# Kernel optimization log

Measured on AMD Instinct MI355X. Metric: run time of the kernel, lower is better.

Reference implementation:

```python
import jax, jax.numpy as jnp
import numpy as np


def setup_inputs() -> dict:
    key = jax.random.key(0)
    k1, k2, k3 = jax.random.split(key, 3)
    B, H, W, C, Q = 32, 64, 64, 256, 4
    h = jax.random.normal(k1, (B, H, W, C), dtype=jnp.float32)
    mask = jax.random.randint(k2, (B, H, W), 0, 2) == 1  # True = masked out
    queries = jax.random.normal(k3, (Q, C), dtype=jnp.float32)
    return {"h": h, "mask": mask, "queries": queries}


def reference(h, mask, queries):
    B, H, W, C = h.shape
    Q = queries.shape[0]
    scale = C ** (-0.5)
    h_flat = h.reshape(B, H * W, C)            # [B, N, C]
    # scores: [B, Q, N]
    attn = jnp.einsum('qc,bnc->bqn', queries, h_flat) * scale
    mask_flat = mask.reshape(B, 1, H * W)      # True -> -inf
    attn = jnp.where(mask_flat, -jnp.inf, attn)
    attn = jax.nn.softmax(attn, axis=-1)
    attn = jnp.where(jnp.isnan(attn), 0.0, attn)  # nan_to_num for fully-masked rows
    pooled = jnp.einsum('bqn,bnc->bqc', attn, h_flat)
    return pooled.reshape(B, Q * C)
```

## Files before the change

### kernel.cpp

```cpp
#include <hip/hip_runtime.h>
#include <math.h>

#define QN  4
#define CN  256
#define BN  32
#define NN  4096
#define WV  4
#define RPW 32
#define TR  4
#define NT  8
#define SPB 32

__global__ __launch_bounds__(256) void k_fused(
    const float* __restrict__ h, const int* __restrict__ mask,
    const float* __restrict__ qr,
    float* __restrict__ P, float* __restrict__ L)
{
    __shared__ float s_part[WV][QN * CN];
    __shared__ float s_lp[WV][QN];

    const int b    = blockIdx.x >> 5;
    const int sub  = blockIdx.x & (SPB - 1);
    const int w    = threadIdx.x >> 6;
    const int lane = threadIdx.x & 63;

    const int n0    = (sub * WV + w) * RPW;
    const size_t gn = (size_t)b * NN + n0;
    const float* __restrict__ hb = h + gn * CN + lane * 4;

    float4 q4[QN];
#pragma unroll
    for (int q = 0; q < QN; ++q) {
        float4 tq = *(const float4*)(qr + q * CN + lane * 4);
        tq.x *= 0.0625f; tq.y *= 0.0625f; tq.z *= 0.0625f; tq.w *= 0.0625f;
        q4[q] = tq;
    }

    const unsigned long long mbits =
        __ballot(lane < RPW ? (mask[gn + lane] != 0) : true);

    float4 acc[QN];
#pragma unroll
    for (int q = 0; q < QN; ++q) acc[q] = make_float4(0.f, 0.f, 0.f, 0.f);

    float lheld = 0.f;
    const int rheld = (lane >> 2) & 3;

    float4 vc[TR], vn[TR];
#pragma unroll
    for (int j = 0; j < TR; ++j) {
        vc[j] = make_float4(0.f, 0.f, 0.f, 0.f);
        vn[j] = make_float4(0.f, 0.f, 0.f, 0.f);
    }
#pragma unroll
    for (int j = 0; j < TR; ++j)
        if (!((mbits >> j) & 1ull))
            vc[j] = *(const float4*)(hb + (size_t)j * CN);

#pragma unroll
    for (int t = 0; t < NT; ++t) {
        if (t + 1 < NT) {
#pragma unroll
            for (int j = 0; j < TR; ++j) {
                const int rw = (t + 1) * TR + j;
                if (!((mbits >> rw) & 1ull))
                    vn[j] = *(const float4*)(hb + (size_t)rw * CN);
            }
        }

        float cur[16];
#pragma unroll
        for (int r = 0; r < TR; ++r)
#pragma unroll
            for (int q = 0; q < QN; ++q)
                cur[r * 4 + q] = vc[r].x * q4[q].x + vc[r].y * q4[q].y
                               + vc[r].z * q4[q].z + vc[r].w * q4[q].w;

#pragma unroll
        for (int k = 0; k < 4; ++k) {
            const int  nv = 8 >> k;
            const bool bk = (lane >> k) & 1;
#pragma unroll
            for (int j = 0; j < nv; ++j) {
                const float snd = bk ? cur[2 * j] : cur[2 * j + 1];
                const float rcv = __shfl_xor(snd, 1 << k, 64);
                cur[j] = (bk ? cur[2 * j + 1] : cur[2 * j]) + rcv;
            }
        }
        float sv = cur[0];
        sv += __shfl_xor(sv, 16, 64);
        sv += __shfl_xor(sv, 32, 64);

        const bool  mk = ((mbits >> (t * TR + rheld)) & 1ull) != 0;
        const float pv = mk ? 0.f : __expf(sv);
        lheld += pv;

#pragma unroll
        for (int r = 0; r < TR; ++r)
#pragma unroll
            for (int q = 0; q < QN; ++q) {
                const float prq = __uint_as_float(
                    __builtin_amdgcn_readlane(__float_as_uint(pv), r * 4 + q));
                acc[q].x += prq * vc[r].x;
                acc[q].y += prq * vc[r].y;
                acc[q].z += prq * vc[r].z;
                acc[q].w += prq * vc[r].w;
            }

#pragma unroll
        for (int j = 0; j < TR; ++j) vc[j] = vn[j];
    }

    float lt = lheld;
    lt += __shfl_xor(lt, 4, 64);
    lt += __shfl_xor(lt, 8, 64);

#pragma unroll
    for (int q = 0; q < QN; ++q)
        *(float4*)&s_part[w][q * CN + lane * 4] = acc[q];
    if (lane < QN) s_lp[w][lane] = lt;
    __syncthreads();
    {
        const int tt = threadIdx.x;
        float4 o = make_float4(0.f, 0.f, 0.f, 0.f);
#pragma unroll
        for (int ww = 0; ww < WV; ++ww) {
            const float4 v = *(const float4*)&s_part[ww][tt * 4];
            o.x += v.x; o.y += v.y; o.z += v.z; o.w += v.w;
        }
        ((float4*)(P + (size_t)blockIdx.x * (QN * CN)))[tt] = o;
        if (tt < QN)
            L[blockIdx.x * QN + tt] =
                s_lp[0][tt] + s_lp[1][tt] + s_lp[2][tt] + s_lp[3][tt];
    }
}

__global__ __launch_bounds__(256) void k_div(
    const float* __restrict__ P, const float* __restrict__ L,
    float* __restrict__ out)
{
    const int b   = blockIdx.x >> 2;
    const int q   = blockIdx.x & 3;
    const int idx = q * CN + threadIdx.x;

    float o = 0.f, l = 0.f;
#pragma unroll 4
    for (int s = 0; s < SPB; ++s) {
        o += P[(size_t)(b * SPB + s) * (QN * CN) + idx];
        l += L[(b * SPB + s) * QN + q];
    }
    out[(size_t)b * (QN * CN) + idx] = (l > 0.f) ? o / l : 0.f;
}

extern "C" void kernel_launch(void* const* d_in, const int* in_sizes, int n_in,
                              void* d_out, int out_size, void* d_ws, size_t ws_size,
                              hipStream_t stream) {
    const float* h    = (const float*)d_in[0];
    const int*   mask = (const int*)d_in[1];
    const float* qr   = (const float*)d_in[2];
    float*       out  = (float*)d_out;

    float* P = (float*)d_ws;
    float* L = P + (size_t)BN * SPB * QN * CN;

    k_fused<<<BN * SPB, 256, 0, stream>>>(h, mask, qr, P, L);
    k_div  <<<BN * QN, 256, 0, stream>>>(P, L, out);
}
```

Baseline: 28.64 us.

## Compact unmasked rows per wave and prefetch two tiles ahead

Instead of iterating over all 32 rows of each wave, including masked ones, the kernel now extracts the indices of unmasked rows from the ballot mask and packs them into dense groups of four. It then runs a dynamic loop over only those groups, so compute and exp on masked rows are skipped. Prefetching deepens from one to two tiles ahead to hide load latency. The trade-off is a runtime loop bound and ctz-based index extraction in place of a fully unrolled static loop, plus extra registers for the third buffer.

```diff
diff --git a/kernel.cpp b/kernel.cpp
--- a/kernel.cpp
+++ b/kernel.cpp
@@ -7,14 +7,25 @@
 #define NN  4096
 #define WV  4
 #define RPW 32
-#define TR  4
-#define NT  8
 #define SPB 32
+
+#define EXTRACT_ISSUE(dst, vmdst) do {                                   \
+    vmdst = 0u;                                                          \
+    _Pragma("unroll")                                                    \
+    for (int j_ = 0; j_ < 4; ++j_) {                                     \
+        if (um) {                                                        \
+            const int r_ = __builtin_ctz(um);                            \
+            um &= um - 1u;                                               \
+            vmdst |= (1u << j_);                                         \
+            dst[j_] = *(const float4*)(hb + (size_t)r_ * CN);            \
+        }                                                                \
+    }                                                                    \
+} while (0)
 
 __global__ __launch_bounds__(256) void k_fused(
     const float* __restrict__ h, const int* __restrict__ mask,
     const float* __restrict__ qr,
-    float* __restrict__ P, float* __restrict__ L)
+    float* __restrict__ P, float* __restrict__ Lp)
 {
     __shared__ float s_part[WV][QN * CN];
     __shared__ float s_lp[WV][QN];
@@ -38,6 +49,9 @@
 
     const unsigned long long mbits =
         __ballot(lane < RPW ? (mask[gn + lane] != 0) : true);
+    unsigned um = (unsigned)(~mbits & 0xFFFFFFFFull);
+    const int K   = __popc(um);
+    const int NTv = (K + 3) >> 2;
 
     float4 acc[QN];
 #pragma unroll
@@ -46,31 +60,25 @@
     float lheld = 0.f;
     const int rheld = (lane >> 2) & 3;
 
-    float4 vc[TR], vn[TR];
+    float4 vc[4], vn[4], vn2[4];
 #pragma unroll
-    for (int j = 0; j < TR; ++j) {
+    for (int j = 0; j < 4; ++j) {
         vc[j] = make_float4(0.f, 0.f, 0.f, 0.f);
         vn[j] = make_float4(0.f, 0.f, 0.f, 0.f);
+        vn2[j] = make_float4(0.f, 0.f, 0.f, 0.f);
     }
-#pragma unroll
-    for (int j = 0; j < TR; ++j)
-        if (!((mbits >> j) & 1ull))
-            vc[j] = *(const float4*)(hb + (size_t)j * CN);
+    unsigned vm0, vm1, vm2;
 
-#pragma unroll
-    for (int t = 0; t < NT; ++t) {
-        if (t + 1 < NT) {
-#pragma unroll
-            for (int j = 0; j < TR; ++j) {
-                const int rw = (t + 1) * TR + j;
-                if (!((mbits >> rw) & 1ull))
-                    vn[j] = *(const float4*)(hb + (size_t)rw * CN);
-            }
-        }
+    EXTRACT_ISSUE(vc, vm0);
+    EXTRACT_ISSUE(vn, vm1);
+
+    for (int t = 0; t < NTv; ++t) {
+        if (t + 2 < NTv) EXTRACT_ISSUE(vn2, vm2);
+        else             vm2 = 0u;
 
         float cur[16];
 #pragma unroll
-        for (int r = 0; r < TR; ++r)
+        for (int r = 0; r < 4; ++r)
 #pragma unroll
             for (int q = 0; q < QN; ++q)
                 cur[r * 4 + q] = vc[r].x * q4[q].x + vc[r].y * q4[q].y
@@ -91,12 +99,12 @@
         sv += __shfl_xor(sv, 16, 64);
         sv += __shfl_xor(sv, 32, 64);
 
-        const bool  mk = ((mbits >> (t * TR + rheld)) & 1ull) != 0;
-        const float pv = mk ? 0.f : __expf(sv);
+        const bool  ok = (vm0 >> rheld) & 1u;
+        const float pv = ok ? __expf(sv) : 0.f;
         lheld += pv;
 
 #pragma unroll
-        for (int r = 0; r < TR; ++r)
+        for (int r = 0; r < 4; ++r)
 #pragma unroll
             for (int q = 0; q < QN; ++q) {
                 const float prq = __uint_as_float(
@@ -108,7 +116,8 @@
             }
 
 #pragma unroll
-        for (int j = 0; j < TR; ++j) vc[j] = vn[j];
+        for (int j = 0; j < 4; ++j) { vc[j] = vn[j]; vn[j] = vn2[j]; }
+        vm0 = vm1; vm1 = vm2;
     }
 
     float lt = lheld;
@@ -130,13 +139,13 @@
         }
         ((float4*)(P + (size_t)blockIdx.x * (QN * CN)))[tt] = o;
         if (tt < QN)
-            L[blockIdx.x * QN + tt] =
+            Lp[blockIdx.x * QN + tt] =
                 s_lp[0][tt] + s_lp[1][tt] + s_lp[2][tt] + s_lp[3][tt];
     }
 }
 
 __global__ __launch_bounds__(256) void k_div(
-    const float* __restrict__ P, const float* __restrict__ L,
+    const float* __restrict__ P, const float* __restrict__ Lp,
     float* __restrict__ out)
 {
     const int b   = blockIdx.x >> 2;
@@ -147,7 +156,7 @@
 #pragma unroll 4
     for (int s = 0; s < SPB; ++s) {
         o += P[(size_t)(b * SPB + s) * (QN * CN) + idx];
-        l += L[(b * SPB + s) * QN + q];
+        l += Lp[(b * SPB + s) * QN + q];
     }
     out[(size_t)b * (QN * CN) + idx] = (l > 0.f) ? o / l : 0.f;
 }
@@ -160,9 +169,9 @@
     const float* qr   = (const float*)d_in[2];
     float*       out  = (float*)d_out;
 
-    float* P = (float*)d_ws;
-    float* L = P + (size_t)BN * SPB * QN * CN;
+    float* P  = (float*)d_ws;
+    float* Lp = P + (size_t)BN * SPB * QN * CN;
 
-    k_fused<<<BN * SPB, 256, 0, stream>>>(h, mask, qr, P, L);
-    k_div  <<<BN * QN, 256, 0, stream>>>(P, L, out);
+    k_fused<<<BN * SPB, 256, 0, stream>>>(h, mask, qr, P, Lp);
+    k_div  <<<BN * QN, 256, 0, stream>>>(P, Lp, out);
 }
```

New measurement: 24.96 us. 12.9% less time.
